# Kernel tuning notes

Hardware: AMD Instinct MI355X
Metric: run time of the kernel (lower is better)

Reference implementation:

```python
import jax, jax.numpy as jnp
import numpy as np

DIM, HEADS, WH, WW, NPROMPT, NW, BATCH = 384, 12, 7, 7, 5, 64, 32
N = WH * WW + NPROMPT  # 54


def _make_rel_index():
    ch, cw = np.meshgrid(np.arange(WH), np.arange(WW), indexing='ij')
    coords = np.stack([ch, cw]).reshape(2, -1)  # [2, 49]
    rel = coords[:, :, None] - coords[:, None, :]  # [2,49,49]
    rel = rel.transpose(1, 2, 0)
    rel[:, :, 0] += WH - 1
    rel[:, :, 1] += WW - 1
    rel[:, :, 0] *= 2 * WW - 1
    return rel.sum(-1).astype(np.int32)  # [49,49]


def setup_inputs() -> dict:
    key = jax.random.key(0)
    ks = jax.random.split(key, 7)
    B_ = BATCH * NW
    x = jax.random.normal(ks[0], (B_, N, DIM), jnp.float32)
    # 0/-inf style shifted-window mask; random floats exercise the same math
    mask = jnp.where(jax.random.uniform(ks[1], (NW, WH * WW, WH * WW)) > 0.8,
                     jnp.float32(-100.0), jnp.float32(0.0))
    qkv_w = 0.02 * jax.random.normal(ks[2], (3 * DIM, DIM), jnp.float32)
    qkv_b = 0.02 * jax.random.normal(ks[3], (3 * DIM,), jnp.float32)
    proj_w = 0.02 * jax.random.normal(ks[4], (DIM, DIM), jnp.float32)
    proj_b = 0.02 * jax.random.normal(ks[5], (DIM,), jnp.float32)
    rpb_table = 0.02 * jax.random.normal(ks[6], ((2 * WH - 1) * (2 * WW - 1), HEADS), jnp.float32)
    rel_index = jnp.asarray(_make_rel_index())
    return {"x": x, "mask": mask, "qkv_w": qkv_w, "qkv_b": qkv_b,
            "proj_w": proj_w, "proj_b": proj_b, "rpb_table": rpb_table,
            "rel_index": rel_index}


def reference(x, mask, qkv_w, qkv_b, proj_w, proj_b, rpb_table, rel_index):
    B_, n, C = x.shape
    hd = C // HEADS
    scale = hd ** -0.5
    qkv = (x @ qkv_w.T + qkv_b).reshape(B_, n, 3, HEADS, hd)
    qkv = jnp.moveaxis(qkv, 2, 0)  # [3, B_, n, H, hd]
    q, k, v = qkv[0], qkv[1], qkv[2]  # [B_, n, H, hd]
    attn = jnp.einsum('bnhd,bmhd->bhnm', q * scale, k)  # [B_, H, n, n]
    nw2 = WH * WW
    bias = rpb_table[rel_index.reshape(-1)].reshape(nw2, nw2, HEADS)
    bias = jnp.transpose(bias, (2, 0, 1))  # [H, 49, 49]
    bias = jnp.pad(bias, ((0, 0), (NPROMPT, 0), (NPROMPT, 0)))  # [H, n, n]
    attn = attn + bias[None]
    nW = mask.shape[0]
    mask_p = jnp.pad(mask, ((0, 0), (NPROMPT, 0), (NPROMPT, 0)))  # [nW, n, n]
    attn = attn.reshape(B_ // nW, nW, HEADS, n, n) + mask_p[None, :, None]
    attn = jax.nn.softmax(attn.reshape(B_, HEADS, n, n), axis=-1)
    out = jnp.einsum('bhnm,bmhd->bnhd', attn, v).reshape(B_, n, C)
    return out @ proj_w.T + proj_b
```

## Files before the change

kernel.cpp:

```cpp
#include <hip/hip_runtime.h>

#define DIM 384
#define NH 12
#define NT 54
#define NWIN 64

typedef __attribute__((ext_vector_type(8))) short short8;
typedef __attribute__((ext_vector_type(4))) float f32x4;

__device__ __forceinline__ unsigned short f2bf(float f) {
  unsigned int u = __float_as_uint(f);
  u += 0x7fffu + ((u >> 16) & 1u);
  return (unsigned short)(u >> 16);
}
__device__ __forceinline__ float bf2f(unsigned short s) {
  return __uint_as_float((unsigned int)s << 16);
}

__global__ __launch_bounds__(256) void convert_x(
    const float* __restrict__ x, unsigned short* __restrict__ xb) {
  const size_t i8 = ((size_t)blockIdx.x * 256 + threadIdx.x) * 8;
  float4 fa = *(const float4*)&x[i8];
  float4 fb = *(const float4*)&x[i8 + 4];
  short8 s;
  s[0] = f2bf(fa.x); s[1] = f2bf(fa.y); s[2] = f2bf(fa.z); s[3] = f2bf(fa.w);
  s[4] = f2bf(fb.x); s[5] = f2bf(fb.y); s[6] = f2bf(fb.z); s[7] = f2bf(fb.w);
  *(short8*)&xb[i8] = s;
}

__global__ __launch_bounds__(256) void prep2_kernel(
    const float* __restrict__ qkv_w, const float* __restrict__ proj_w,
    const float* __restrict__ mask, const float* __restrict__ rpb,
    const int* __restrict__ rel,
    unsigned short* __restrict__ Wq, unsigned short* __restrict__ Wp,
    unsigned short* __restrict__ bmt) {
  int idx = blockIdx.x * 256 + threadIdx.x;
  if (idx < 1152 * 384) { Wq[idx] = f2bf(qkv_w[idx]); return; }
  idx -= 1152 * 384;
  if (idx < 384 * 384) { Wp[idx] = f2bf(proj_w[idx]); return; }
  idx -= 384 * 384;
  if (idx < NWIN * NH * 64 * 64) {
    int w = idx / (NH * 4096);
    int rem = idx - w * (NH * 4096);
    int h = rem >> 12, r = (rem >> 6) & 63, c = rem & 63;
    float v;
    if (r >= NT || c >= NT) v = -1e30f;
    else if (r >= 5 && c >= 5)
      v = rpb[rel[(r - 5) * 49 + (c - 5)] * NH + h] +
          mask[w * 2401 + (r - 5) * 49 + (c - 5)];
    else v = 0.0f;
    bmt[w * (NH * 4096) + (h << 12) + (c << 6) + r] = f2bf(v);
  }
}

__global__ __launch_bounds__(256) void qkv_gemm2(
    const unsigned short* __restrict__ xb, const unsigned short* __restrict__ Wq,
    const float* __restrict__ qkv_b, unsigned short* __restrict__ QKVb) {
  __shared__ unsigned short As[128][72];
  __shared__ unsigned short Bs[128][72];
  const int s = blockIdx.x;
  const int xcd = s & 7, slot = s >> 3;
  const size_t m0 = (size_t)(xcd * 108 + slot / 9) * 128;
  const int n0 = (slot % 9) * 128;
  const int tid = threadIdx.x;
  const int wv = tid >> 6, ln = tid & 63, g = ln >> 4, lc = ln & 15;
  const int wr = (wv >> 1) * 64, wc = (wv & 1) * 64;
  f32x4 acc[4][4];
#pragma unroll
  for (int i = 0; i < 4; ++i)
#pragma unroll
    for (int j = 0; j < 4; ++j) acc[i][j] = (f32x4){0.f, 0.f, 0.f, 0.f};

  const int srow = tid >> 3, l8 = tid & 7;
  for (int kc = 0; kc < 6; ++kc) {
    const int k0 = kc * 64;
#pragma unroll
    for (int it = 0; it < 4; ++it) {
      const int r = srow + it * 32;
      *(short8*)&As[r][l8 * 8] =
          *(const short8*)&xb[(m0 + r) * 384 + k0 + l8 * 8];
      *(short8*)&Bs[r][l8 * 8] =
          *(const short8*)&Wq[(size_t)(n0 + r) * 384 + k0 + l8 * 8];
    }
    __syncthreads();
#pragma unroll
    for (int kk = 0; kk < 2; ++kk) {
      short8 af[4], bfr[4];
#pragma unroll
      for (int ms = 0; ms < 4; ++ms)
        af[ms] = *(const short8*)&As[wr + ms * 16 + lc][kk * 32 + g * 8];
#pragma unroll
      for (int ns = 0; ns < 4; ++ns)
        bfr[ns] = *(const short8*)&Bs[wc + ns * 16 + lc][kk * 32 + g * 8];
#pragma unroll
      for (int ms = 0; ms < 4; ++ms)
#pragma unroll
        for (int ns = 0; ns < 4; ++ns)
          acc[ms][ns] = __builtin_amdgcn_mfma_f32_16x16x32_bf16(
              af[ms], bfr[ns], acc[ms][ns], 0, 0, 0);
    }
    __syncthreads();
  }
  const float factor = (n0 < 384) ? 0.17677669529663687f : 1.0f;
#pragma unroll
  for (int ns = 0; ns < 4; ++ns) {
    const int n = n0 + wc + ns * 16 + lc;
    const float bias = qkv_b[n];
#pragma unroll
    for (int ms = 0; ms < 4; ++ms)
#pragma unroll
      for (int rr = 0; rr < 4; ++rr) {
        const size_t m = m0 + wr + ms * 16 + g * 4 + rr;
        QKVb[m * 1152 + n] = f2bf((acc[ms][ns][rr] + bias) * factor);
      }
  }
}

__global__ __launch_bounds__(256) void attn2_kernel(
    unsigned short* __restrict__ QKVb, const unsigned short* __restrict__ bmt) {
  __shared__ unsigned short Ps[NT][72];
  __shared__ unsigned short vT[32][72];
  const int s = blockIdx.x;
  const int xcd = s & 7, slot = s >> 3;
  const int b = xcd * 256 + slot / 12;
  const int h = slot - 12 * (slot / 12);
  const int tid = threadIdx.x;
  const int wv = tid >> 6, ln = tid & 63, g = ln >> 4, lc = ln & 15;
  const int m0 = wv * 16, wi = b & 63;
  const size_t base = (size_t)b * NT;
  const int arow = (m0 + lc < NT) ? (m0 + lc) : (NT - 1);

  for (int i = tid; i < 320; i += 256) {
    int d = i / 10, m = NT + (i - d * 10);
    vT[d][m] = 0;
  }

  const int vr = tid >> 2, vc = (tid & 3) * 8;
  short8 vv;
  if (tid < 216)
    vv = *(const short8*)&QKVb[(base + vr) * 1152 + 768 + h * 32 + vc];

  short8 a = *(const short8*)&QKVb[(base + arow) * 1152 + h * 32 + g * 8];
  const unsigned short* bmh = &bmt[(size_t)(wi * NH + h) << 12];
  const int row0 = m0 + g * 4;
  f32x4 sac[4];
#pragma unroll
  for (int t = 0; t < 4; ++t) {
    const int col = t * 16 + lc;
    const int kr = (col < NT) ? col : (NT - 1);
    short8 kb = *(const short8*)&QKVb[(base + kr) * 1152 + 384 + h * 32 + g * 8];
    uint2 uu = *(const uint2*)&bmh[(col << 6) + row0];
    f32x4 c0;
    c0[0] = bf2f((unsigned short)(uu.x & 0xffffu));
    c0[1] = bf2f((unsigned short)(uu.x >> 16));
    c0[2] = bf2f((unsigned short)(uu.y & 0xffffu));
    c0[3] = bf2f((unsigned short)(uu.y >> 16));
    sac[t] = __builtin_amdgcn_mfma_f32_16x16x32_bf16(a, kb, c0, 0, 0, 0);
  }
  float rmax[4] = {-3.0e38f, -3.0e38f, -3.0e38f, -3.0e38f};
#pragma unroll
  for (int t = 0; t < 4; ++t)
#pragma unroll
    for (int rr = 0; rr < 4; ++rr) rmax[rr] = fmaxf(rmax[rr], sac[t][rr]);
#pragma unroll
  for (int rr = 0; rr < 4; ++rr)
#pragma unroll
    for (int off = 1; off < 16; off <<= 1)
      rmax[rr] = fmaxf(rmax[rr], __shfl_xor(rmax[rr], off));
  float rsum[4] = {0.f, 0.f, 0.f, 0.f};
#pragma unroll
  for (int t = 0; t < 4; ++t)
#pragma unroll
    for (int rr = 0; rr < 4; ++rr) {
      float p = __expf(sac[t][rr] - rmax[rr]);
      sac[t][rr] = p;
      rsum[rr] += p;
    }
#pragma unroll
  for (int rr = 0; rr < 4; ++rr) {
#pragma unroll
    for (int off = 1; off < 16; off <<= 1)
      rsum[rr] += __shfl_xor(rsum[rr], off);
    rsum[rr] = 1.0f / rsum[rr];
  }
#pragma unroll
  for (int t = 0; t < 4; ++t)
#pragma unroll
    for (int rr = 0; rr < 4; ++rr) {
      const int row = row0 + rr;
      if (row < NT) Ps[row][t * 16 + lc] = f2bf(sac[t][rr] * rsum[rr]);
    }
  if (tid < 216) {
#pragma unroll
    for (int j = 0; j < 8; ++j) vT[vc + j][vr] = (unsigned short)vv[j];
  }
  __syncthreads();
  f32x4 oac[2];
  oac[0] = (f32x4){0.f, 0.f, 0.f, 0.f};
  oac[1] = (f32x4){0.f, 0.f, 0.f, 0.f};
#pragma unroll
  for (int k2 = 0; k2 < 2; ++k2) {
    short8 pa = *(const short8*)&Ps[arow][k2 * 32 + g * 8];
#pragma unroll
    for (int tn = 0; tn < 2; ++tn) {
      short8 vb = *(const short8*)&vT[tn * 16 + lc][k2 * 32 + g * 8];
      oac[tn] = __builtin_amdgcn_mfma_f32_16x16x32_bf16(pa, vb, oac[tn], 0, 0, 0);
    }
  }
#pragma unroll
  for (int tn = 0; tn < 2; ++tn) {
    const int d = tn * 16 + lc;
#pragma unroll
    for (int rr = 0; rr < 4; ++rr) {
      const int m = m0 + g * 4 + rr;
      if (m < NT) QKVb[(base + m) * 1152 + h * 32 + d] = f2bf(oac[tn][rr]);
    }
  }
}

__global__ __launch_bounds__(256) void proj_kernel(
    const unsigned short* __restrict__ AO, const unsigned short* __restrict__ Wp,
    const float* __restrict__ proj_b, float* __restrict__ out, int lda) {
  __shared__ unsigned short As[128][72];
  __shared__ unsigned short Bs[128][72];
  const int s = blockIdx.x;
  const int xcd = s & 7, slot = s >> 3;
  const size_t m0 = (size_t)(xcd * 108 + slot / 3) * 128;
  const int n0 = (slot % 3) * 128;
  const int tid = threadIdx.x;
  const int wv = tid >> 6, ln = tid & 63, g = ln >> 4, lc = ln & 15;
  const int wr = (wv >> 1) * 64, wc = (wv & 1) * 64;
  f32x4 acc[4][4];
#pragma unroll
  for (int i = 0; i < 4; ++i)
#pragma unroll
    for (int j = 0; j < 4; ++j) acc[i][j] = (f32x4){0.f, 0.f, 0.f, 0.f};

  const int srow = tid >> 3, l8 = tid & 7;
  for (int kc = 0; kc < 6; ++kc) {
    const int k0 = kc * 64;
#pragma unroll
    for (int it = 0; it < 4; ++it) {
      const int r = srow + it * 32;
      *(short8*)&As[r][l8 * 8] =
          *(const short8*)&AO[(m0 + r) * (size_t)lda + k0 + l8 * 8];
      *(short8*)&Bs[r][l8 * 8] =
          *(const short8*)&Wp[(size_t)(n0 + r) * 384 + k0 + l8 * 8];
    }
    __syncthreads();
#pragma unroll
    for (int kk = 0; kk < 2; ++kk) {
      short8 af[4], bfr[4];
#pragma unroll
      for (int ms = 0; ms < 4; ++ms)
        af[ms] = *(const short8*)&As[wr + ms * 16 + lc][kk * 32 + g * 8];
#pragma unroll
      for (int ns = 0; ns < 4; ++ns)
        bfr[ns] = *(const short8*)&Bs[wc + ns * 16 + lc][kk * 32 + g * 8];
#pragma unroll
      for (int ms = 0; ms < 4; ++ms)
#pragma unroll
        for (int ns = 0; ns < 4; ++ns)
          acc[ms][ns] = __builtin_amdgcn_mfma_f32_16x16x32_bf16(
              af[ms], bfr[ns], acc[ms][ns], 0, 0, 0);
    }
    __syncthreads();
  }
#pragma unroll
  for (int ns = 0; ns < 4; ++ns) {
    const int n = n0 + wc + ns * 16 + lc;
    const float pb = proj_b[n];
#pragma unroll
    for (int ms = 0; ms < 4; ++ms)
#pragma unroll
      for (int rr = 0; rr < 4; ++rr) {
        const size_t m = m0 + wr + ms * 16 + g * 4 + rr;
        out[m * 384 + n] = acc[ms][ns][rr] + pb;
      }
  }
}

__global__ __launch_bounds__(256) void prep_kernel(
    const float* __restrict__ qkv_w, const float* __restrict__ proj_w,
    const float* __restrict__ mask, const float* __restrict__ rpb,
    const int* __restrict__ rel,
    unsigned short* __restrict__ Wq, unsigned short* __restrict__ Wp,
    float* __restrict__ bias_tab, float* __restrict__ maskp) {
  int idx = blockIdx.x * 256 + threadIdx.x;
  if (idx < 1152 * 384) { Wq[idx] = f2bf(qkv_w[idx]); return; }
  idx -= 1152 * 384;
  if (idx < 384 * 384) { Wp[idx] = f2bf(proj_w[idx]); return; }
  idx -= 384 * 384;
  if (idx < NH * 64 * 64) {
    int h = idx >> 12, r = (idx >> 6) & 63, c = idx & 63;
    float v;
    if (r >= NT || c >= NT) v = -1e30f;
    else if (r >= 5 && c >= 5) v = rpb[rel[(r - 5) * 49 + (c - 5)] * NH + h];
    else v = 0.0f;
    bias_tab[idx] = v;
    return;
  }
  idx -= NH * 64 * 64;
  if (idx < NWIN * 64 * 64) {
    int w = idx >> 12, r = (idx >> 6) & 63, c = idx & 63;
    float v = 0.0f;
    if (r >= 5 && r < NT && c >= 5 && c < NT)
      v = mask[w * 2401 + (r - 5) * 49 + (c - 5)];
    maskp[idx] = v;
  }
}

__global__ __launch_bounds__(256) void fused_attn(
    const float* __restrict__ x, const unsigned short* __restrict__ Wq,
    const float* __restrict__ qkv_b, const float* __restrict__ bias_tab,
    const float* __restrict__ maskp, unsigned short* __restrict__ AO) {
  __shared__ unsigned short xs[NT][392];
  __shared__ unsigned short qs[NT][40];
  __shared__ unsigned short ksm[NT][40];
  __shared__ unsigned short vT[32][72];
  __shared__ unsigned short Ps[NT][72];
  const int b = blockIdx.x;
  const int tid = threadIdx.x;
  const int wv = tid >> 6, ln = tid & 63;
  const int g = ln >> 4, lc = ln & 15;
  const int m0 = wv * 16;
  const int wi = b & 63;
  const float scale = 0.17677669529663687f;
  const float* xb = x + (size_t)b * (NT * DIM);
  for (int i = tid; i < NT * DIM / 4; i += 256) {
    float4 v = ((const float4*)xb)[i];
    int e = i * 4, r = e / DIM, c = e - r * DIM;
    unsigned short* p = &xs[r][c];
    p[0] = f2bf(v.x); p[1] = f2bf(v.y); p[2] = f2bf(v.z); p[3] = f2bf(v.w);
  }
  __syncthreads();
  const int arow = (m0 + lc < NT) ? (m0 + lc) : (NT - 1);
  for (int h = 0; h < NH; ++h) {
    f32x4 acc[6];
#pragma unroll
    for (int t = 0; t < 6; ++t) acc[t] = (f32x4){0.f, 0.f, 0.f, 0.f};
#pragma unroll 2
    for (int kk = 0; kk < 12; ++kk) {
      short8 a = *(const short8*)&xs[arow][kk * 32 + g * 8];
#pragma unroll
      for (int t = 0; t < 6; ++t) {
        const int sel = t >> 1;
        const int wrow = sel * 384 + h * 32 + (t & 1) * 16 + lc;
        short8 bfr = *(const short8*)&Wq[wrow * 384 + kk * 32 + g * 8];
        acc[t] = __builtin_amdgcn_mfma_f32_16x16x32_bf16(a, bfr, acc[t], 0, 0, 0);
      }
    }
#pragma unroll
    for (int t = 0; t < 6; ++t) {
      const int sel = t >> 1;
      const int d = (t & 1) * 16 + lc;
      const float bias = qkv_b[sel * 384 + h * 32 + d];
#pragma unroll
      for (int r = 0; r < 4; ++r) {
        const int m = m0 + g * 4 + r;
        float v = acc[t][r] + bias;
        if (sel == 2) vT[d][m] = f2bf(v);
        else if (m < NT) {
          if (sel == 0) qs[m][d] = f2bf(v * scale);
          else ksm[m][d] = f2bf(v);
        }
      }
    }
    __syncthreads();
    f32x4 sac[4];
    {
      short8 a = *(const short8*)&qs[arow][g * 8];
#pragma unroll
      for (int t = 0; t < 4; ++t) {
        const int kr = (t * 16 + lc < NT) ? (t * 16 + lc) : (NT - 1);
        short8 bfr = *(const short8*)&ksm[kr][g * 8];
        sac[t] = __builtin_amdgcn_mfma_f32_16x16x32_bf16(
            a, bfr, (f32x4){0.f, 0.f, 0.f, 0.f}, 0, 0, 0);
      }
    }
    const float* bt = bias_tab + h * 4096;
    const float* mp = maskp + wi * 4096;
    float sv[4][4];
    float rmax[4];
#pragma unroll
    for (int r = 0; r < 4; ++r) rmax[r] = -3.0e38f;
#pragma unroll
    for (int t = 0; t < 4; ++t) {
      const int col = t * 16 + lc;
#pragma unroll
      for (int r = 0; r < 4; ++r) {
        const int row = m0 + g * 4 + r;
        float s = sac[t][r] + bt[row * 64 + col] + mp[row * 64 + col];
        sv[t][r] = s;
        rmax[r] = fmaxf(rmax[r], s);
      }
    }
#pragma unroll
    for (int r = 0; r < 4; ++r)
#pragma unroll
      for (int off = 1; off < 16; off <<= 1)
        rmax[r] = fmaxf(rmax[r], __shfl_xor(rmax[r], off));
    float rsum[4] = {0.f, 0.f, 0.f, 0.f};
#pragma unroll
    for (int t = 0; t < 4; ++t)
#pragma unroll
      for (int r = 0; r < 4; ++r) {
        float p = __expf(sv[t][r] - rmax[r]);
        sv[t][r] = p;
        rsum[r] += p;
      }
#pragma unroll
    for (int r = 0; r < 4; ++r) {
#pragma unroll
      for (int off = 1; off < 16; off <<= 1)
        rsum[r] += __shfl_xor(rsum[r], off);
      rsum[r] = 1.0f / rsum[r];
    }
#pragma unroll
    for (int t = 0; t < 4; ++t) {
      const int col = t * 16 + lc;
#pragma unroll
      for (int r = 0; r < 4; ++r) {
        const int row = m0 + g * 4 + r;
        if (row < NT) Ps[row][col] = f2bf(sv[t][r] * rsum[r]);
      }
    }
    __syncthreads();
    f32x4 oac[2];
    oac[0] = (f32x4){0.f, 0.f, 0.f, 0.f};
    oac[1] = (f32x4){0.f, 0.f, 0.f, 0.f};
#pragma unroll
    for (int k2 = 0; k2 < 2; ++k2) {
      short8 a = *(const short8*)&Ps[arow][k2 * 32 + g * 8];
#pragma unroll
      for (int tn = 0; tn < 2; ++tn) {
        short8 bfr = *(const short8*)&vT[tn * 16 + lc][k2 * 32 + g * 8];
        oac[tn] = __builtin_amdgcn_mfma_f32_16x16x32_bf16(a, bfr, oac[tn], 0, 0, 0);
      }
    }
    unsigned short* aob = AO + (size_t)b * (NT * DIM) + h * 32;
#pragma unroll
    for (int tn = 0; tn < 2; ++tn) {
      const int d = tn * 16 + lc;
#pragma unroll
      for (int r = 0; r < 4; ++r) {
        const int m = m0 + g * 4 + r;
        if (m < NT) aob[m * DIM + d] = f2bf(oac[tn][r]);
      }
    }
    __syncthreads();
  }
}

extern "C" void kernel_launch(void* const* d_in, const int* in_sizes, int n_in,
                              void* d_out, int out_size, void* d_ws, size_t ws_size,
                              hipStream_t stream) {
  const float* x      = (const float*)d_in[0];
  const float* mask   = (const float*)d_in[1];
  const float* qkv_w  = (const float*)d_in[2];
  const float* qkv_b  = (const float*)d_in[3];
  const float* proj_w = (const float*)d_in[4];
  const float* proj_b = (const float*)d_in[5];
  const float* rpb    = (const float*)d_in[6];
  const int*   rel    = (const int*)d_in[7];
  float* out = (float*)d_out;

  const size_t M = 110592;
  const size_t QKV_ELEMS = M * 1152;
  const size_t WQ_ELEMS = 1152 * 384, WP_ELEMS = 384 * 384;
  const size_t BMT_ELEMS = (size_t)NWIN * NH * 4096;
  const size_t need = (QKV_ELEMS + WQ_ELEMS + WP_ELEMS + BMT_ELEMS) * 2;

  if (ws_size >= need) {
    unsigned short* QKVb = (unsigned short*)d_ws;
    unsigned short* Wq   = QKVb + QKV_ELEMS;
    unsigned short* Wp   = Wq + WQ_ELEMS;
    unsigned short* bmt  = Wp + WP_ELEMS;
    unsigned short* xb = (unsigned short*)d_out;

    convert_x<<<20736, 256, 0, stream>>>(x, xb);
    prep2_kernel<<<14592, 256, 0, stream>>>(qkv_w, proj_w, mask, rpb, rel,
                                            Wq, Wp, bmt);
    qkv_gemm2<<<7776, 256, 0, stream>>>(xb, Wq, qkv_b, QKVb);
    attn2_kernel<<<24576, 256, 0, stream>>>(QKVb, bmt);
    proj_kernel<<<2592, 256, 0, stream>>>(QKVb, Wp, proj_b, out, 1152);
  } else {
    unsigned short* Wq = (unsigned short*)d_ws;
    unsigned short* Wp = Wq + 442368;
    float* bias_tab = (float*)(Wp + 147456);
    float* maskp = bias_tab + 12 * 64 * 64;
    unsigned short* AO = (unsigned short*)(maskp + 64 * 64 * 64);
    prep_kernel<<<3520, 256, 0, stream>>>(qkv_w, proj_w, mask, rpb, rel,
                                          Wq, Wp, bias_tab, maskp);
    fused_attn<<<2048, 256, 0, stream>>>(x, Wq, qkv_b, bias_tab, maskp, AO);
    proj_kernel<<<2592, 256, 0, stream>>>(AO, Wp, proj_b, out, 384);
  }
}
```

Baseline: 436.4 us.

## Store Q/K/V in head-major layout so attention reads contiguous per-head tiles

The QKV GEMM epilogue now writes Q, K and V into separate head-major buffers ([head][token][32]) instead of one interleaved [token][1152] array. The attention kernel then reads each head's 54x32 slice as one contiguous block, and the projection GEMM gathers its A operand from the head-major attention output. This aims to improve coalescing and cache-line use in the attention loads. In exchange, the QKV epilogue writes 64-byte runs instead of longer rows, and the projection loads now span several head planes.

```diff
diff --git a/kernel.cpp b/kernel.cpp
--- a/kernel.cpp
+++ b/kernel.cpp
@@ -4,6 +4,8 @@
 #define NH 12
 #define NT 54
 #define NWIN 64
+#define MTOT 110592
+#define HS ((size_t)MTOT * 32)
 
 typedef __attribute__((ext_vector_type(8))) short short8;
 typedef __attribute__((ext_vector_type(4))) float f32x4;
@@ -55,7 +57,9 @@
 
 __global__ __launch_bounds__(256) void qkv_gemm2(
     const unsigned short* __restrict__ xb, const unsigned short* __restrict__ Wq,
-    const float* __restrict__ qkv_b, unsigned short* __restrict__ QKVb) {
+    const float* __restrict__ qkv_b,
+    unsigned short* __restrict__ Qb, unsigned short* __restrict__ Kb,
+    unsigned short* __restrict__ Vb) {
   __shared__ unsigned short As[128][72];
   __shared__ unsigned short Bs[128][72];
   const int s = blockIdx.x;
@@ -101,23 +105,28 @@
     }
     __syncthreads();
   }
-  const float factor = (n0 < 384) ? 0.17677669529663687f : 1.0f;
+  const int sel = n0 / 384;
+  const float factor = (sel == 0) ? 0.17677669529663687f : 1.0f;
+  unsigned short* outp = (sel == 0) ? Qb : (sel == 1 ? Kb : Vb);
 #pragma unroll
   for (int ns = 0; ns < 4; ++ns) {
     const int n = n0 + wc + ns * 16 + lc;
+    const int rel = n - sel * 384;
+    const int h = rel >> 5, d = rel & 31;
     const float bias = qkv_b[n];
 #pragma unroll
     for (int ms = 0; ms < 4; ++ms)
 #pragma unroll
       for (int rr = 0; rr < 4; ++rr) {
         const size_t m = m0 + wr + ms * 16 + g * 4 + rr;
-        QKVb[m * 1152 + n] = f2bf((acc[ms][ns][rr] + bias) * factor);
+        outp[(size_t)h * HS + m * 32 + d] = f2bf((acc[ms][ns][rr] + bias) * factor);
       }
   }
 }
 
 __global__ __launch_bounds__(256) void attn2_kernel(
-    unsigned short* __restrict__ QKVb, const unsigned short* __restrict__ bmt) {
+    unsigned short* __restrict__ Qb, const unsigned short* __restrict__ Kb,
+    const unsigned short* __restrict__ Vb, const unsigned short* __restrict__ bmt) {
   __shared__ unsigned short Ps[NT][72];
   __shared__ unsigned short vT[32][72];
   const int s = blockIdx.x;
@@ -129,6 +138,9 @@
   const int m0 = wv * 16, wi = b & 63;
   const size_t base = (size_t)b * NT;
   const int arow = (m0 + lc < NT) ? (m0 + lc) : (NT - 1);
+  unsigned short* Qh = Qb + (size_t)h * HS;
+  const unsigned short* Kh = Kb + (size_t)h * HS;
+  const unsigned short* Vh = Vb + (size_t)h * HS;
 
   for (int i = tid; i < 320; i += 256) {
     int d = i / 10, m = NT + (i - d * 10);
@@ -138,9 +150,9 @@
   const int vr = tid >> 2, vc = (tid & 3) * 8;
   short8 vv;
   if (tid < 216)
-    vv = *(const short8*)&QKVb[(base + vr) * 1152 + 768 + h * 32 + vc];
-
-  short8 a = *(const short8*)&QKVb[(base + arow) * 1152 + h * 32 + g * 8];
+    vv = *(const short8*)&Vh[(base + vr) * 32 + vc];
+
+  short8 a = *(const short8*)&Qh[(base + arow) * 32 + g * 8];
   const unsigned short* bmh = &bmt[(size_t)(wi * NH + h) << 12];
   const int row0 = m0 + g * 4;
   f32x4 sac[4];
@@ -148,7 +160,7 @@
   for (int t = 0; t < 4; ++t) {
     const int col = t * 16 + lc;
     const int kr = (col < NT) ? col : (NT - 1);
-    short8 kb = *(const short8*)&QKVb[(base + kr) * 1152 + 384 + h * 32 + g * 8];
+    short8 kb = *(const short8*)&Kh[(base + kr) * 32 + g * 8];
     uint2 uu = *(const uint2*)&bmh[(col << 6) + row0];
     f32x4 c0;
     c0[0] = bf2f((unsigned short)(uu.x & 0xffffu));
@@ -213,14 +225,14 @@
 #pragma unroll
     for (int rr = 0; rr < 4; ++rr) {
       const int m = m0 + g * 4 + rr;
-      if (m < NT) QKVb[(base + m) * 1152 + h * 32 + d] = f2bf(oac[tn][rr]);
-    }
-  }
-}
-
-__global__ __launch_bounds__(256) void proj_kernel(
+      if (m < NT) Qh[(base + m) * 32 + d] = f2bf(oac[tn][rr]);
+    }
+  }
+}
+
+__global__ __launch_bounds__(256) void proj_hmajor(
     const unsigned short* __restrict__ AO, const unsigned short* __restrict__ Wp,
-    const float* __restrict__ proj_b, float* __restrict__ out, int lda) {
+    const float* __restrict__ proj_b, float* __restrict__ out) {
   __shared__ unsigned short As[128][72];
   __shared__ unsigned short Bs[128][72];
   const int s = blockIdx.x;
@@ -239,11 +251,13 @@
   const int srow = tid >> 3, l8 = tid & 7;
   for (int kc = 0; kc < 6; ++kc) {
     const int k0 = kc * 64;
+    const int kg = k0 + l8 * 8;
+    const int hh = kg >> 5, dd = kg & 31;
 #pragma unroll
     for (int it = 0; it < 4; ++it) {
       const int r = srow + it * 32;
       *(short8*)&As[r][l8 * 8] =
-          *(const short8*)&AO[(m0 + r) * (size_t)lda + k0 + l8 * 8];
+          *(const short8*)&AO[(size_t)hh * HS + (m0 + r) * 32 + dd];
       *(short8*)&Bs[r][l8 * 8] =
           *(const short8*)&Wp[(size_t)(n0 + r) * 384 + k0 + l8 * 8];
     }
@@ -452,6 +466,68 @@
   }
 }
 
+__global__ __launch_bounds__(256) void proj_kernel(
+    const unsigned short* __restrict__ AO, const unsigned short* __restrict__ Wp,
+    const float* __restrict__ proj_b, float* __restrict__ out, int lda) {
+  __shared__ unsigned short As[128][72];
+  __shared__ unsigned short Bs[128][72];
+  const int s = blockIdx.x;
+  const int xcd = s & 7, slot = s >> 3;
+  const size_t m0 = (size_t)(xcd * 108 + slot / 3) * 128;
+  const int n0 = (slot % 3) * 128;
+  const int tid = threadIdx.x;
+  const int wv = tid >> 6, ln = tid & 63, g = ln >> 4, lc = ln & 15;
+  const int wr = (wv >> 1) * 64, wc = (wv & 1) * 64;
+  f32x4 acc[4][4];
+#pragma unroll
+  for (int i = 0; i < 4; ++i)
+#pragma unroll
+    for (int j = 0; j < 4; ++j) acc[i][j] = (f32x4){0.f, 0.f, 0.f, 0.f};
+
+  const int srow = tid >> 3, l8 = tid & 7;
+  for (int kc = 0; kc < 6; ++kc) {
+    const int k0 = kc * 64;
+#pragma unroll
+    for (int it = 0; it < 4; ++it) {
+      const int r = srow + it * 32;
+      *(short8*)&As[r][l8 * 8] =
+          *(const short8*)&AO[(m0 + r) * (size_t)lda + k0 + l8 * 8];
+      *(short8*)&Bs[r][l8 * 8] =
+          *(const short8*)&Wp[(size_t)(n0 + r) * 384 + k0 + l8 * 8];
+    }
+    __syncthreads();
+#pragma unroll
+    for (int kk = 0; kk < 2; ++kk) {
+      short8 af[4], bfr[4];
+#pragma unroll
+      for (int ms = 0; ms < 4; ++ms)
+        af[ms] = *(const short8*)&As[wr + ms * 16 + lc][kk * 32 + g * 8];
+#pragma unroll
+      for (int ns = 0; ns < 4; ++ns)
+        bfr[ns] = *(const short8*)&Bs[wc + ns * 16 + lc][kk * 32 + g * 8];
+#pragma unroll
+      for (int ms = 0; ms < 4; ++ms)
+#pragma unroll
+        for (int ns = 0; ns < 4; ++ns)
+          acc[ms][ns] = __builtin_amdgcn_mfma_f32_16x16x32_bf16(
+              af[ms], bfr[ns], acc[ms][ns], 0, 0, 0);
+    }
+    __syncthreads();
+  }
+#pragma unroll
+  for (int ns = 0; ns < 4; ++ns) {
+    const int n = n0 + wc + ns * 16 + lc;
+    const float pb = proj_b[n];
+#pragma unroll
+    for (int ms = 0; ms < 4; ++ms)
+#pragma unroll
+      for (int rr = 0; rr < 4; ++rr) {
+        const size_t m = m0 + wr + ms * 16 + g * 4 + rr;
+        out[m * 384 + n] = acc[ms][ns][rr] + pb;
+      }
+  }
+}
+
 extern "C" void kernel_launch(void* const* d_in, const int* in_sizes, int n_in,
                               void* d_out, int out_size, void* d_ws, size_t ws_size,
                               hipStream_t stream) {
@@ -465,25 +541,26 @@
   const int*   rel    = (const int*)d_in[7];
   float* out = (float*)d_out;
 
-  const size_t M = 110592;
-  const size_t QKV_ELEMS = M * 1152;
+  const size_t QKV_ELEMS = (size_t)3 * NH * HS;
   const size_t WQ_ELEMS = 1152 * 384, WP_ELEMS = 384 * 384;
   const size_t BMT_ELEMS = (size_t)NWIN * NH * 4096;
   const size_t need = (QKV_ELEMS + WQ_ELEMS + WP_ELEMS + BMT_ELEMS) * 2;
 
   if (ws_size >= need) {
-    unsigned short* QKVb = (unsigned short*)d_ws;
-    unsigned short* Wq   = QKVb + QKV_ELEMS;
-    unsigned short* Wp   = Wq + WQ_ELEMS;
-    unsigned short* bmt  = Wp + WP_ELEMS;
+    unsigned short* Qb  = (unsigned short*)d_ws;
+    unsigned short* Kb  = Qb + NH * HS;
+    unsigned short* Vb  = Kb + NH * HS;
+    unsigned short* Wq  = Vb + NH * HS;
+    unsigned short* Wp  = Wq + WQ_ELEMS;
+    unsigned short* bmt = Wp + WP_ELEMS;
     unsigned short* xb = (unsigned short*)d_out;
 
     convert_x<<<20736, 256, 0, stream>>>(x, xb);
     prep2_kernel<<<14592, 256, 0, stream>>>(qkv_w, proj_w, mask, rpb, rel,
                                             Wq, Wp, bmt);
-    qkv_gemm2<<<7776, 256, 0, stream>>>(xb, Wq, qkv_b, QKVb);
-    attn2_kernel<<<24576, 256, 0, stream>>>(QKVb, bmt);
-    proj_kernel<<<2592, 256, 0, stream>>>(QKVb, Wp, proj_b, out, 1152);
+    qkv_gemm2<<<7776, 256, 0, stream>>>(xb, Wq, qkv_b, Qb, Kb, Vb);
+    attn2_kernel<<<24576, 256, 0, stream>>>(Qb, Kb, Vb, bmt);
+    proj_hmajor<<<2592, 256, 0, stream>>>(Qb, Wp, proj_b, out);
   } else {
     unsigned short* Wq = (unsigned short*)d_ws;
     unsigned short* Wp = Wq + 442368;
```

Result: faster. 419.8 us (-3.8%).
